# Performance work log

Measured on AMD Instinct MI355X. Metric: run time of the kernel, lower is better.

The kernel has to match this reference:

```python
import jax, jax.numpy as jnp
import numpy as np

B, S, D_MODEL, D_FORWARD, HEAD = 4, 2048, 1024, 1024, 16
D_K = D_FORWARD // HEAD


def setup_inputs() -> dict:
    key = jax.random.key(0)
    ks = jax.random.split(key, 6)
    scale = 1.0 / np.sqrt(D_MODEL)
    x = jax.random.normal(ks[0], (B, S, D_MODEL), dtype=jnp.float32)
    # per-head projection weights, PyTorch Linear layout [out, in] stacked over heads
    Wq = jax.random.normal(ks[1], (HEAD, D_K, D_MODEL), dtype=jnp.float32) * scale
    Wk = jax.random.normal(ks[2], (HEAD, D_K, D_MODEL), dtype=jnp.float32) * scale
    Wv = jax.random.normal(ks[3], (HEAD, D_K, D_MODEL), dtype=jnp.float32) * scale
    Wo = jax.random.normal(ks[4], (D_MODEL, D_FORWARD), dtype=jnp.float32) * (1.0 / np.sqrt(D_FORWARD))
    bo = jax.random.normal(ks[5], (D_MODEL,), dtype=jnp.float32) * 0.01
    return {"x": x, "Wq": Wq, "Wk": Wk, "Wv": Wv, "Wo": Wo, "bo": bo}


def reference(x, Wq, Wk, Wv, Wo, bo):
    d_k = Wq.shape[1]
    # fused per-head projections: q,k,v are [B, H, S, d_k]
    q = jnp.einsum("bsm,hkm->bhsk", x, Wq)
    k = jnp.einsum("bsm,hkm->bhsk", x, Wk)
    v = jnp.einsum("bsm,hkm->bhsk", x, Wv)
    # raw scores [B, H, S, S]
    scores = jnp.einsum("bhqd,bhkd->bhqk", q, k)
    # custom zero-value mask: entries that are exactly 0 get -1e9
    scores = jnp.where(scores != 0, scores, jnp.float32(-1e9))
    # NOTE: original divides by scale_factor = d_k**-0.5, i.e. multiplies by sqrt(d_k)
    att = jax.nn.softmax(scores * jnp.sqrt(jnp.float32(d_k)), axis=-1)
    z = jnp.einsum("bhqk,bhkd->bhqd", att, v)  # [B, H, S, d_k]
    n_batch, h, s, _ = z.shape
    z = jnp.transpose(z, (0, 2, 1, 3)).reshape(n_batch, s, h * d_k)  # [B, S, d_forward]
    return z @ Wo.T + bo
```

## Files before the change

### kernel.cpp

```cpp
#include <hip/hip_runtime.h>
#include <stdint.h>

typedef __attribute__((ext_vector_type(4))) float f32x4;
typedef __attribute__((ext_vector_type(8))) _Float16 half8;
typedef __attribute__((ext_vector_type(4))) unsigned int u32x4;
typedef __attribute__((ext_vector_type(2))) unsigned int u32x2;

#define MFMA_F16(a, b, c) __builtin_amdgcn_mfma_f32_16x16x32_f16(a, b, c, 0, 0, 0)

#define GLD16(gp, lp)                                                          \
  __builtin_amdgcn_global_load_lds(                                            \
      (const __attribute__((address_space(1))) void*)(gp),                     \
      (__attribute__((address_space(3))) void*)(lp), 16, 0, 0)

__device__ __forceinline__ short f2h(float f) {
  union { _Float16 h; short s; } v;
  v.h = (_Float16)f;
  return v.s;
}
__device__ __forceinline__ float exp2_hw(float x) {
  float r;
  asm("v_exp_f32 %0, %1" : "=v"(r) : "v"(x));
  return r;
}
__device__ __forceinline__ uint32_t pkhf(float lo, float hi) {
  uint32_t r;
  asm("v_cvt_pkrtz_f16_f32 %0, %1, %2" : "=v"(r) : "v"(lo), "v"(hi));
  return r;
}

__global__ __launch_bounds__(256) void cast4_f16(const float* __restrict__ src,
                                                 short* __restrict__ d, int n4) {
  int i = blockIdx.x * 256 + threadIdx.x;
  if (i < n4) {
    f32x4 v = *reinterpret_cast<const f32x4*>(src + (size_t)i * 4);
    u32x2 o;
    o[0] = pkhf(v[0], v[1]);
    o[1] = pkhf(v[2], v[3]);
    *reinterpret_cast<u32x2*>(d + (size_t)i * 4) = o;
  }
}

__global__ __launch_bounds__(256) void gemm_proj(
    const short* __restrict__ Xf, const short* __restrict__ Wf,
    short* __restrict__ Qf, short* __restrict__ Kf, short* __restrict__ Vt) {
  __shared__ short sA[128 * 32], sB[128 * 32];
  const int tid = threadIdx.x, lane = tid & 63, w = tid >> 6;
  const int wr = w >> 1, wc = w & 1;
  const int g = lane >> 4, c = lane & 15;
  const int m0 = blockIdx.y * 128, n0 = blockIdx.x * 128;

  f32x4 acc[4][4];
#pragma unroll
  for (int i = 0; i < 4; i++)
#pragma unroll
    for (int j = 0; j < 4; j++) acc[i][j] = (f32x4){0.f, 0.f, 0.f, 0.f};

  const int swG = (g ^ ((c >> 1) & 3)) * 8;

  for (int ks = 0; ks < 32; ks++) {
    const int k0 = ks * 32;
    __syncthreads();
#pragma unroll
    for (int i = 0; i < 2; i++) {
      const int chunk = i * 256 + w * 64 + lane;
      const int row = chunk >> 2;
      const int colg = (chunk & 3) ^ ((row >> 1) & 3);
      const size_t aoff = (size_t)(m0 + row) * 1024 + k0 + colg * 8;
      const size_t boff = (size_t)(n0 + row) * 1024 + k0 + colg * 8;
      const int ldsoff = chunk * 16;
      GLD16(Xf + aoff, (char*)sA + ldsoff);
      GLD16(Wf + boff, (char*)sB + ldsoff);
    }
    asm volatile("s_waitcnt vmcnt(0)" ::: "memory");
    __syncthreads();

    half8 a[4], b8[4];
#pragma unroll
    for (int i = 0; i < 4; i++) {
      a[i] = *(const half8*)&sA[(wr * 64 + i * 16 + c) * 32 + swG];
      b8[i] = *(const half8*)&sB[(wc * 64 + i * 16 + c) * 32 + swG];
    }
#pragma unroll
    for (int i = 0; i < 4; i++)
#pragma unroll
      for (int j = 0; j < 4; j++) acc[i][j] = MFMA_F16(a[i], b8[j], acc[i][j]);
  }

  const int section = n0 >> 10;
#pragma unroll
  for (int i = 0; i < 4; i++)
#pragma unroll
    for (int j = 0; j < 4; j++)
#pragma unroll
      for (int r = 0; r < 4; r++) {
        const float v = acc[i][j][r];
        const int m = m0 + wr * 64 + i * 16 + g * 4 + r;
        const int n = n0 + wc * 64 + j * 16 + c;
        const int b = m >> 11, s = m & 2047;
        const int nn = n & 1023;
        const int hh = nn >> 6, d = nn & 63;
        if (section == 0) {
          const size_t off = ((size_t)(b * 16 + hh) * 2048 + s) * 64 + d;
          Qf[off] = f2h(v * 11.5415603271f);
        } else if (section == 1) {
          const size_t off = ((size_t)(b * 16 + hh) * 2048 + s) * 64 + d;
          Kf[off] = f2h(v);
        } else {
          Vt[((size_t)(b * 16 + hh) * 64 + d) * 2048 + s] = f2h(v);
        }
      }
}

__global__ __launch_bounds__(256, 4) void attn_kernel(
    const short* __restrict__ Qf, const short* __restrict__ Kf,
    const short* __restrict__ Vt, short* __restrict__ Z) {
  __shared__ short sK[2][64 * 64];
  __shared__ short sV[2][64 * 64];
  const int tid = threadIdx.x, lane = tid & 63, w = tid >> 6;
  const int g = lane >> 4, c = lane & 15;
  const int L = blockIdx.x;
  const int wid = (L & 7) * 128 + (L >> 3);
  const int qblk = wid & 15, bh = wid >> 4;
  const int b = bh >> 4, h = bh & 15;
  const size_t base = (size_t)bh * (2048 * 64);

  half8 qf[2][2];
  {
    const int qrow = qblk * 128 + w * 32 + c;
#pragma unroll
    for (int qi = 0; qi < 2; qi++)
#pragma unroll
      for (int cc = 0; cc < 2; cc++) {
        const size_t off =
            base + (size_t)(qrow + qi * 16) * 64 + cc * 32 + g * 8;
        qf[qi][cc] = *(const half8*)(Qf + off);
      }
  }

  f32x4 zacc[2][4];
  f32x4 lacc[2];
  float m_run[2] = {-INFINITY, -INFINITY};
#pragma unroll
  for (int qi = 0; qi < 2; qi++) {
    lacc[qi] = (f32x4){0.f, 0.f, 0.f, 0.f};
#pragma unroll
    for (int dt = 0; dt < 4; dt++) zacc[qi][dt] = (f32x4){0.f, 0.f, 0.f, 0.f};
  }

  half8 ones;
#pragma unroll
  for (int i = 0; i < 8; i++) ones[i] = (_Float16)1.0f;

  const int sw0 = ((0 * 4 + g) ^ (c & 7)) * 8;
  const int sw1 = ((1 * 4 + g) ^ (c & 7)) * 8;

  const int ch0 = tid, ch1 = tid + 256;
  const int kr0 = ch0 >> 3, kc0 = (ch0 & 7) ^ (kr0 & 7);
  const int kr1 = ch1 >> 3, kc1 = (ch1 & 7) ^ (kr1 & 7);
  const int kofs0 = kr0 * 64 + kc0 * 8, kofs1 = kr1 * 64 + kc1 * 8;
  const int vofs0 = kr0 * 2048 + kc0 * 8, vofs1 = kr1 * 2048 + kc1 * 8;
  const int ldo0 = ch0 * 16, ldo1 = ch1 * 16;

  auto stage = [&](int buf, int kt) {
    const size_t kb = base + (size_t)kt * 4096;
    const size_t vb = base + (size_t)kt * 64;
    GLD16(Kf + kb + kofs0, (char*)&sK[buf][0] + ldo0);
    GLD16(Kf + kb + kofs1, (char*)&sK[buf][0] + ldo1);
    GLD16(Vt + vb + vofs0, (char*)&sV[buf][0] + ldo0);
    GLD16(Vt + vb + vofs1, (char*)&sV[buf][0] + ldo1);
  };

  const int srcl = ((g & 1) << 5) + c;

  auto compute = [&](int buf) {
    f32x4 sacc[2][4];
#pragma unroll
    for (int qi = 0; qi < 2; qi++)
#pragma unroll
      for (int t = 0; t < 4; t++) sacc[qi][t] = (f32x4){0.f, 0.f, 0.f, 0.f};
    __builtin_amdgcn_s_setprio(1);
#pragma unroll
    for (int cc = 0; cc < 2; cc++) {
      const int sw = cc ? sw1 : sw0;
#pragma unroll
      for (int t = 0; t < 4; t++) {
        const int kr = (t * 16 + c) * 64 + sw;
        half8 k8 = *(const half8*)&sK[buf][kr];
        sacc[0][t] = MFMA_F16(k8, qf[0][cc], sacc[0][t]);
        sacc[1][t] = MFMA_F16(k8, qf[1][cc], sacc[1][t]);
      }
    }
    __builtin_amdgcn_s_setprio(0);

    float p0[16], p1[16];
#pragma unroll
    for (int t = 0; t < 4; t++)
#pragma unroll
      for (int r = 0; r < 4; r++) {
        p0[t * 4 + r] = sacc[0][t][r];
        p1[t * 4 + r] = sacc[1][t][r];
      }
    float mx0, mx1;
    {
      float a = fmaxf(fmaxf(fmaxf(p0[0], p0[1]), fmaxf(p0[2], p0[3])),
                      fmaxf(fmaxf(p0[4], p0[5]), fmaxf(p0[6], p0[7])));
      float bq = fmaxf(fmaxf(fmaxf(p0[8], p0[9]), fmaxf(p0[10], p0[11])),
                       fmaxf(fmaxf(p0[12], p0[13]), fmaxf(p0[14], p0[15])));
      mx0 = fmaxf(a, bq);
      mx0 = fmaxf(mx0, __shfl_xor(mx0, 16));
      mx0 = fmaxf(mx0, __shfl_xor(mx0, 32));
    }
    {
      float a = fmaxf(fmaxf(fmaxf(p1[0], p1[1]), fmaxf(p1[2], p1[3])),
                      fmaxf(fmaxf(p1[4], p1[5]), fmaxf(p1[6], p1[7])));
      float bq = fmaxf(fmaxf(fmaxf(p1[8], p1[9]), fmaxf(p1[10], p1[11])),
                       fmaxf(fmaxf(p1[12], p1[13]), fmaxf(p1[14], p1[15])));
      mx1 = fmaxf(a, bq);
      mx1 = fmaxf(mx1, __shfl_xor(mx1, 16));
      mx1 = fmaxf(mx1, __shfl_xor(mx1, 32));
    }
    const float growmax = fmaxf(mx0 - m_run[0], mx1 - m_run[1]);
    if (__any(growmax > 8.0f)) {
#pragma unroll
      for (int qi = 0; qi < 2; qi++) {
        const float mnew = fmaxf(m_run[qi], qi ? mx1 : mx0);
        const float sc = exp2_hw(m_run[qi] - mnew);
        m_run[qi] = mnew;
#pragma unroll
        for (int r = 0; r < 4; r++) lacc[qi][r] *= sc;
#pragma unroll
        for (int dt = 0; dt < 4; dt++)
#pragma unroll
          for (int r = 0; r < 4; r++) zacc[qi][dt][r] *= sc;
      }
    }
#pragma unroll
    for (int i = 0; i < 16; i++) {
      p0[i] = exp2_hw(p0[i] - m_run[0]);
      p1[i] = exp2_hw(p1[i] - m_run[1]);
    }

    union { u32x4 u; half8 s; } pfa0, pfa1, pfb0, pfb1;
    {
      const uint32_t wA0 = pkhf(p0[0], p0[1]), wA1 = pkhf(p0[2], p0[3]);
      const uint32_t wB0 = pkhf(p0[4], p0[5]), wB1 = pkhf(p0[6], p0[7]);
      const uint32_t a0 = __shfl(wA0, srcl), a1 = __shfl(wA1, srcl);
      const uint32_t b0 = __shfl(wB0, srcl), b1 = __shfl(wB1, srcl);
      const uint32_t a2 = __shfl(wA0, srcl + 16), a3 = __shfl(wA1, srcl + 16);
      const uint32_t b2 = __shfl(wB0, srcl + 16), b3 = __shfl(wB1, srcl + 16);
      pfa0.u[0] = (g < 2) ? a0 : b0;
      pfa0.u[1] = (g < 2) ? a1 : b1;
      pfa0.u[2] = (g < 2) ? a2 : b2;
      pfa0.u[3] = (g < 2) ? a3 : b3;
    }
    {
      const uint32_t wA0 = pkhf(p0[8], p0[9]), wA1 = pkhf(p0[10], p0[11]);
      const uint32_t wB0 = pkhf(p0[12], p0[13]), wB1 = pkhf(p0[14], p0[15]);
      const uint32_t a0 = __shfl(wA0, srcl), a1 = __shfl(wA1, srcl);
      const uint32_t b0 = __shfl(wB0, srcl), b1 = __shfl(wB1, srcl);
      const uint32_t a2 = __shfl(wA0, srcl + 16), a3 = __shfl(wA1, srcl + 16);
      const uint32_t b2 = __shfl(wB0, srcl + 16), b3 = __shfl(wB1, srcl + 16);
      pfa1.u[0] = (g < 2) ? a0 : b0;
      pfa1.u[1] = (g < 2) ? a1 : b1;
      pfa1.u[2] = (g < 2) ? a2 : b2;
      pfa1.u[3] = (g < 2) ? a3 : b3;
    }
    {
      const uint32_t wA0 = pkhf(p1[0], p1[1]), wA1 = pkhf(p1[2], p1[3]);
      const uint32_t wB0 = pkhf(p1[4], p1[5]), wB1 = pkhf(p1[6], p1[7]);
      const uint32_t a0 = __shfl(wA0, srcl), a1 = __shfl(wA1, srcl);
      const uint32_t b0 = __shfl(wB0, srcl), b1 = __shfl(wB1, srcl);
      const uint32_t a2 = __shfl(wA0, srcl + 16), a3 = __shfl(wA1, srcl + 16);
      const uint32_t b2 = __shfl(wB0, srcl + 16), b3 = __shfl(wB1, srcl + 16);
      pfb0.u[0] = (g < 2) ? a0 : b0;
      pfb0.u[1] = (g < 2) ? a1 : b1;
      pfb0.u[2] = (g < 2) ? a2 : b2;
      pfb0.u[3] = (g < 2) ? a3 : b3;
    }
    {
      const uint32_t wA0 = pkhf(p1[8], p1[9]), wA1 = pkhf(p1[10], p1[11]);
      const uint32_t wB0 = pkhf(p1[12], p1[13]), wB1 = pkhf(p1[14], p1[15]);
      const uint32_t a0 = __shfl(wA0, srcl), a1 = __shfl(wA1, srcl);
      const uint32_t b0 = __shfl(wB0, srcl), b1 = __shfl(wB1, srcl);
      const uint32_t a2 = __shfl(wA0, srcl + 16), a3 = __shfl(wA1, srcl + 16);
      const uint32_t b2 = __shfl(wB0, srcl + 16), b3 = __shfl(wB1, srcl + 16);
      pfb1.u[0] = (g < 2) ? a0 : b0;
      pfb1.u[1] = (g < 2) ? a1 : b1;
      pfb1.u[2] = (g < 2) ? a2 : b2;
      pfb1.u[3] = (g < 2) ? a3 : b3;
    }

    __builtin_amdgcn_s_setprio(1);
    lacc[0] = MFMA_F16(ones, pfa0.s, lacc[0]);
    lacc[0] = MFMA_F16(ones, pfa1.s, lacc[0]);
    lacc[1] = MFMA_F16(ones, pfb0.s, lacc[1]);
    lacc[1] = MFMA_F16(ones, pfb1.s, lacc[1]);
#pragma unroll
    for (int dt = 0; dt < 4; dt++) {
      const int vr = (dt * 16 + c) * 64;
      half8 vb0 = *(const half8*)&sV[buf][vr + sw0];
      half8 vb1 = *(const half8*)&sV[buf][vr + sw1];
      zacc[0][dt] = MFMA_F16(vb0, pfa0.s, zacc[0][dt]);
      zacc[0][dt] = MFMA_F16(vb1, pfa1.s, zacc[0][dt]);
      zacc[1][dt] = MFMA_F16(vb0, pfb0.s, zacc[1][dt]);
      zacc[1][dt] = MFMA_F16(vb1, pfb1.s, zacc[1][dt]);
    }
    __builtin_amdgcn_s_setprio(0);
  };

  stage(0, 0);
  asm volatile("s_waitcnt vmcnt(0)" ::: "memory");
  __builtin_amdgcn_s_barrier();

#pragma unroll 1
  for (int t2 = 0; t2 < 16; t2++) {
    {
      stage(1, 2 * t2 + 1);
      compute(0);
      asm volatile("s_waitcnt vmcnt(0) lgkmcnt(0)" ::: "memory");
      __builtin_amdgcn_s_barrier();
    }
    {
      const int nxt = 2 * t2 + 2;
      stage(0, nxt < 32 ? nxt : 31);
      compute(1);
      asm volatile("s_waitcnt vmcnt(0) lgkmcnt(0)" ::: "memory");
      __builtin_amdgcn_s_barrier();
    }
  }

  const int qg0 = qblk * 128 + w * 32 + c;
#pragma unroll
  for (int qi = 0; qi < 2; qi++) {
    const float rs = lacc[qi][0];
    const float inv = rs > 0.f ? 1.0f / rs : 0.f;
    const int qg = qg0 + qi * 16;
#pragma unroll
    for (int dt = 0; dt < 4; dt++) {
      u32x2 zw;
      zw[0] = pkhf(zacc[qi][dt][0] * inv, zacc[qi][dt][1] * inv);
      zw[1] = pkhf(zacc[qi][dt][2] * inv, zacc[qi][dt][3] * inv);
      *reinterpret_cast<u32x2*>(
          &Z[(size_t)(b * 2048 + qg) * 1024 + h * 64 + dt * 16 + g * 4]) = zw;
    }
  }
}

__global__ __launch_bounds__(256) void gemm_out(
    const short* __restrict__ Zb, const short* __restrict__ Wof,
    const float* __restrict__ bo, float* __restrict__ out) {
  __shared__ short sA[128 * 32], sB[128 * 32];
  const int tid = threadIdx.x, lane = tid & 63, w = tid >> 6;
  const int wr = w >> 1, wc = w & 1;
  const int g = lane >> 4, c = lane & 15;
  const int m0 = blockIdx.y * 128, n0 = blockIdx.x * 128;

  f32x4 acc[4][4];
#pragma unroll
  for (int i = 0; i < 4; i++)
#pragma unroll
    for (int j = 0; j < 4; j++) acc[i][j] = (f32x4){0.f, 0.f, 0.f, 0.f};

  const int swG = (g ^ ((c >> 1) & 3)) * 8;

  for (int ks = 0; ks < 32; ks++) {
    const int k0 = ks * 32;
    __syncthreads();
#pragma unroll
    for (int i = 0; i < 2; i++) {
      const int chunk = i * 256 + w * 64 + lane;
      const int row = chunk >> 2;
      const int colg = (chunk & 3) ^ ((row >> 1) & 3);
      const size_t aoff = (size_t)(m0 + row) * 1024 + k0 + colg * 8;
      const size_t boff = (size_t)(n0 + row) * 1024 + k0 + colg * 8;
      const int ldsoff = chunk * 16;
      GLD16(Zb + aoff, (char*)sA + ldsoff);
      GLD16(Wof + boff, (char*)sB + ldsoff);
    }
    asm volatile("s_waitcnt vmcnt(0)" ::: "memory");
    __syncthreads();

    half8 a[4], b8[4];
#pragma unroll
    for (int i = 0; i < 4; i++) {
      a[i] = *(const half8*)&sA[(wr * 64 + i * 16 + c) * 32 + swG];
      b8[i] = *(const half8*)&sB[(wc * 64 + i * 16 + c) * 32 + swG];
    }
#pragma unroll
    for (int i = 0; i < 4; i++)
#pragma unroll
      for (int j = 0; j < 4; j++) acc[i][j] = MFMA_F16(a[i], b8[j], acc[i][j]);
  }

#pragma unroll
  for (int i = 0; i < 4; i++)
#pragma unroll
    for (int j = 0; j < 4; j++)
#pragma unroll
      for (int r = 0; r < 4; r++) {
        const int m = m0 + wr * 64 + i * 16 + g * 4 + r;
        const int n = n0 + wc * 64 + j * 16 + c;
        out[(size_t)m * 1024 + n] = acc[i][j][r] + bo[n];
      }
}

extern "C" void kernel_launch(void* const* d_in, const int* in_sizes, int n_in,
                              void* d_out, int out_size, void* d_ws, size_t ws_size,
                              hipStream_t stream) {
  const float* x  = (const float*)d_in[0];
  const float* Wq = (const float*)d_in[1];
  const float* Wk = (const float*)d_in[2];
  const float* Wv = (const float*)d_in[3];
  const float* Wo = (const float*)d_in[4];
  const float* bo = (const float*)d_in[5];
  float* out = (float*)d_out;

  const size_t NX = 8388608;
  const size_t NW = 1048576;
  const size_t NQ = 8388608;

  char* p = (char*)d_ws;
  auto take = [&](size_t bytes) -> char* {
    char* r = p;
    p += (bytes + 255) & ~(size_t)255;
    return r;
  };
  short* Xf  = (short*)take(NX * 2);
  short* Wf  = (short*)take(3 * NW * 2);
  short* Wof = (short*)take(NW * 2);
  short* Qf  = (short*)take(NQ * 2);
  short* Kf  = (short*)take(NQ * 2);
  short* Vt  = (short*)take(NQ * 2);
  short* Zb  = (short*)take(NQ * 2);

  cast4_f16<<<dim3((int)(NX / 1024)), 256, 0, stream>>>(x, Xf, (int)(NX / 4));
  cast4_f16<<<dim3((int)(NW / 1024)), 256, 0, stream>>>(Wq, Wf, (int)(NW / 4));
  cast4_f16<<<dim3((int)(NW / 1024)), 256, 0, stream>>>(Wk, Wf + NW, (int)(NW / 4));
  cast4_f16<<<dim3((int)(NW / 1024)), 256, 0, stream>>>(Wv, Wf + 2 * NW, (int)(NW / 4));
  cast4_f16<<<dim3((int)(NW / 1024)), 256, 0, stream>>>(Wo, Wof, (int)(NW / 4));

  gemm_proj<<<dim3(24, 64), 256, 0, stream>>>(Xf, Wf, Qf, Kf, Vt);
  attn_kernel<<<dim3(1024), 256, 0, stream>>>(Qf, Kf, Vt, Zb);
  gemm_out<<<dim3(8, 64), 256, 0, stream>>>(Zb, Wof, bo, out);
}
```

Baseline: 240.6 us.

## Merge cast kernels into one launch and remap GEMM blocks for XCD locality

Replaces five separate fp32-to-fp16 cast launches with a single kernel that picks its source and destination by block index, removing launch overhead and tail gaps. The projection GEMM grid becomes 1D, with a swizzle that keeps groups of three adjacent column tiles on the same XCD (block index mod 8), aiming for better L2 reuse of weight tiles. The output GEMM also moves to a 1D grid. The softmax row-max reduction is rewritten from a tree into a linear chain, which may lengthen the dependency chain slightly.

Result: no change. 239.8 us (-0.3%).

```diff
diff --git a/kernel.cpp b/kernel.cpp
--- a/kernel.cpp
+++ b/kernel.cpp
@@ -29,16 +29,32 @@
   return r;
 }
 
-__global__ __launch_bounds__(256) void cast4_f16(const float* __restrict__ src,
-                                                 short* __restrict__ d, int n4) {
-  int i = blockIdx.x * 256 + threadIdx.x;
-  if (i < n4) {
-    f32x4 v = *reinterpret_cast<const f32x4*>(src + (size_t)i * 4);
-    u32x2 o;
-    o[0] = pkhf(v[0], v[1]);
-    o[1] = pkhf(v[2], v[3]);
-    *reinterpret_cast<u32x2*>(d + (size_t)i * 4) = o;
-  }
+__global__ __launch_bounds__(256) void cast_all(
+    const float* __restrict__ x, const float* __restrict__ wq,
+    const float* __restrict__ wk, const float* __restrict__ wv,
+    const float* __restrict__ wo, short* __restrict__ Xf,
+    short* __restrict__ Wf, short* __restrict__ Wof) {
+  const int bid = blockIdx.x;
+  const float* src;
+  short* dst;
+  int lb;
+  if (bid < 8192) {
+    src = x; dst = Xf; lb = bid;
+  } else if (bid < 9216) {
+    src = wq; dst = Wf; lb = bid - 8192;
+  } else if (bid < 10240) {
+    src = wk; dst = Wf + 1048576; lb = bid - 9216;
+  } else if (bid < 11264) {
+    src = wv; dst = Wf + 2097152; lb = bid - 10240;
+  } else {
+    src = wo; dst = Wof; lb = bid - 11264;
+  }
+  const size_t i = (size_t)lb * 256 + threadIdx.x;
+  f32x4 v = *reinterpret_cast<const f32x4*>(src + i * 4);
+  u32x2 o;
+  o[0] = pkhf(v[0], v[1]);
+  o[1] = pkhf(v[2], v[3]);
+  *reinterpret_cast<u32x2*>(dst + i * 4) = o;
 }
 
 __global__ __launch_bounds__(256) void gemm_proj(
@@ -48,7 +64,11 @@
   const int tid = threadIdx.x, lane = tid & 63, w = tid >> 6;
   const int wr = w >> 1, wc = w & 1;
   const int g = lane >> 4, c = lane & 15;
-  const int m0 = blockIdx.y * 128, n0 = blockIdx.x * 128;
+  const int L = blockIdx.x;
+  const int xcd = L & 7, idx = L >> 3;
+  const int xcol = xcd * 3 + (idx % 3);
+  const int yrow = idx / 3;
+  const int m0 = yrow * 128, n0 = xcol * 128;
 
   f32x4 acc[4][4];
 #pragma unroll
@@ -203,22 +223,28 @@
       }
     float mx0, mx1;
     {
-      float a = fmaxf(fmaxf(fmaxf(p0[0], p0[1]), fmaxf(p0[2], p0[3])),
-                      fmaxf(fmaxf(p0[4], p0[5]), fmaxf(p0[6], p0[7])));
-      float bq = fmaxf(fmaxf(fmaxf(p0[8], p0[9]), fmaxf(p0[10], p0[11])),
-                       fmaxf(fmaxf(p0[12], p0[13]), fmaxf(p0[14], p0[15])));
-      mx0 = fmaxf(a, bq);
-      mx0 = fmaxf(mx0, __shfl_xor(mx0, 16));
-      mx0 = fmaxf(mx0, __shfl_xor(mx0, 32));
-    }
-    {
-      float a = fmaxf(fmaxf(fmaxf(p1[0], p1[1]), fmaxf(p1[2], p1[3])),
-                      fmaxf(fmaxf(p1[4], p1[5]), fmaxf(p1[6], p1[7])));
-      float bq = fmaxf(fmaxf(fmaxf(p1[8], p1[9]), fmaxf(p1[10], p1[11])),
-                       fmaxf(fmaxf(p1[12], p1[13]), fmaxf(p1[14], p1[15])));
-      mx1 = fmaxf(a, bq);
-      mx1 = fmaxf(mx1, __shfl_xor(mx1, 16));
-      mx1 = fmaxf(mx1, __shfl_xor(mx1, 32));
+      float m = fmaxf(p0[0], p0[1]);
+      m = fmaxf(fmaxf(m, p0[2]), p0[3]);
+      m = fmaxf(fmaxf(m, p0[4]), p0[5]);
+      m = fmaxf(fmaxf(m, p0[6]), p0[7]);
+      m = fmaxf(fmaxf(m, p0[8]), p0[9]);
+      m = fmaxf(fmaxf(m, p0[10]), p0[11]);
+      m = fmaxf(fmaxf(m, p0[12]), p0[13]);
+      m = fmaxf(fmaxf(m, p0[14]), p0[15]);
+      m = fmaxf(m, __shfl_xor(m, 16));
+      mx0 = fmaxf(m, __shfl_xor(m, 32));
+    }
+    {
+      float m = fmaxf(p1[0], p1[1]);
+      m = fmaxf(fmaxf(m, p1[2]), p1[3]);
+      m = fmaxf(fmaxf(m, p1[4]), p1[5]);
+      m = fmaxf(fmaxf(m, p1[6]), p1[7]);
+      m = fmaxf(fmaxf(m, p1[8]), p1[9]);
+      m = fmaxf(fmaxf(m, p1[10]), p1[11]);
+      m = fmaxf(fmaxf(m, p1[12]), p1[13]);
+      m = fmaxf(fmaxf(m, p1[14]), p1[15]);
+      m = fmaxf(m, __shfl_xor(m, 16));
+      mx1 = fmaxf(m, __shfl_xor(m, 32));
     }
     const float growmax = fmaxf(mx0 - m_run[0], mx1 - m_run[1]);
     if (__any(growmax > 8.0f)) {
@@ -354,7 +380,8 @@
   const int tid = threadIdx.x, lane = tid & 63, w = tid >> 6;
   const int wr = w >> 1, wc = w & 1;
   const int g = lane >> 4, c = lane & 15;
-  const int m0 = blockIdx.y * 128, n0 = blockIdx.x * 128;
+  const int L = blockIdx.x;
+  const int m0 = (L >> 3) * 128, n0 = (L & 7) * 128;
 
   f32x4 acc[4][4];
 #pragma unroll
@@ -434,13 +461,8 @@
   short* Vt  = (short*)take(NQ * 2);
   short* Zb  = (short*)take(NQ * 2);
 
-  cast4_f16<<<dim3((int)(NX / 1024)), 256, 0, stream>>>(x, Xf, (int)(NX / 4));
-  cast4_f16<<<dim3((int)(NW / 1024)), 256, 0, stream>>>(Wq, Wf, (int)(NW / 4));
-  cast4_f16<<<dim3((int)(NW / 1024)), 256, 0, stream>>>(Wk, Wf + NW, (int)(NW / 4));
-  cast4_f16<<<dim3((int)(NW / 1024)), 256, 0, stream>>>(Wv, Wf + 2 * NW, (int)(NW / 4));
-  cast4_f16<<<dim3((int)(NW / 1024)), 256, 0, stream>>>(Wo, Wof, (int)(NW / 4));
-
-  gemm_proj<<<dim3(24, 64), 256, 0, stream>>>(Xf, Wf, Qf, Kf, Vt);
+  cast_all<<<dim3(12288), 256, 0, stream>>>(x, Wq, Wk, Wv, Wo, Xf, Wf, Wof);
+  gemm_proj<<<dim3(1536), 256, 0, stream>>>(Xf, Wf, Qf, Kf, Vt);
   attn_kernel<<<dim3(1024), 256, 0, stream>>>(Qf, Kf, Vt, Zb);
-  gemm_out<<<dim3(8, 64), 256, 0, stream>>>(Zb, Wof, bo, out);
-}
+  gemm_out<<<dim3(512), 256, 0, stream>>>(Zb, Wof, bo, out);
+}
```
